# Kernel tuning notes

Hardware: AMD Instinct MI355X
Metric: run time of the kernel (lower is better)

The kernel has to match this reference:

```python
import jax, jax.numpy as jnp
import numpy as np

HEADS = 4
HID = 32
IN = 128
OUT = 8
N = 50000
E = 1600000


def setup_inputs() -> dict:
    key = jax.random.key(0)
    ks = jax.random.split(key, 12)
    x = jax.random.normal(ks[0], (N, IN), dtype=jnp.float32)
    edge_index = jax.random.randint(ks[1], (2, E), 0, N, dtype=jnp.int64)
    s = 0.05
    W1 = jax.random.normal(ks[2], (IN, HEADS * HID), dtype=jnp.float32) * s
    att_src1 = jax.random.normal(ks[3], (HEADS, HID), dtype=jnp.float32) * s
    att_dst1 = jax.random.normal(ks[4], (HEADS, HID), dtype=jnp.float32) * s
    b1 = jnp.zeros((HEADS * HID,), dtype=jnp.float32)
    W2 = jax.random.normal(ks[5], (HEADS * HID, HEADS * HID), dtype=jnp.float32) * s
    att_src2 = jax.random.normal(ks[6], (HEADS, HID), dtype=jnp.float32) * s
    att_dst2 = jax.random.normal(ks[7], (HEADS, HID), dtype=jnp.float32) * s
    b2 = jnp.zeros((HEADS * HID,), dtype=jnp.float32)
    Wout = jax.random.normal(ks[8], (HEADS * HID, OUT), dtype=jnp.float32) * s
    bout = jnp.zeros((OUT,), dtype=jnp.float32)
    return {"x": x, "edge_index": edge_index, "W1": W1, "att_src1": att_src1,
            "att_dst1": att_dst1, "b1": b1, "W2": W2, "att_src2": att_src2,
            "att_dst2": att_dst2, "b2": b2, "Wout": Wout, "bout": bout}


def gat_conv(x, src, dst, W, att_src, att_dst, b):
    n = x.shape[0]
    h = (x @ W).reshape(n, HEADS, HID)              # [N,H,C]
    a_s = (h * att_src).sum(-1)                      # [N,H]
    a_d = (h * att_dst).sum(-1)                      # [N,H]
    e = jax.nn.leaky_relu(a_s[src] + a_d[dst], 0.2)  # [E,H]
    # scatter-softmax over incoming edges of each destination node
    m = jax.ops.segment_max(e, dst, num_segments=n)
    e = jnp.exp(e - m[dst])
    denom = jax.ops.segment_sum(e, dst, num_segments=n)
    alpha = e / (denom[dst] + 1e-16)                 # [E,H]
    msg = h[src] * alpha[:, :, None]                 # [E,H,C]
    out = jax.ops.segment_sum(msg, dst, num_segments=n)
    return out.reshape(n, HEADS * HID) + b


def reference(x, edge_index, W1, att_src1, att_dst1, b1, W2, att_src2, att_dst2, b2, Wout, bout):
    n = x.shape[0]
    # GATConv adds self-loops by default
    loops = jnp.arange(n, dtype=edge_index.dtype)
    src = jnp.concatenate([edge_index[0], loops])
    dst = jnp.concatenate([edge_index[1], loops])
    # dropout p=0.6 is identity in eval mode
    h = gat_conv(x, src, dst, W1, att_src1, att_dst1, b1)
    h = jax.nn.elu(h)
    h = gat_conv(h, src, dst, W2, att_src2, att_dst2, b2)
    return h @ Wout + bout
```

## Files before the change

### kernel.cpp

```cpp
#include <hip/hip_runtime.h>
#include <hip/hip_fp16.h>
#include <math.h>

#define N_NODES 50000
#define E_EDGES 1600000
#define NE_TOT  (E_EDGES + N_NODES)

#define BSH 7
#define NBKT ((N_NODES + 127) >> 7)
#define EPW 4096
#define NWA ((NE_TOT + EPW - 1) / EPW)

#define CH 128


__global__ __launch_bounds__(256) void k_binhist(const int* __restrict__ ei,
                                                 int* __restrict__ histG) {
    __shared__ int h[NBKT];
    int t = threadIdx.x;
    for (int i = t; i < NBKT; i += 256) h[i] = 0;
    __syncthreads();
    int base = blockIdx.x * EPW;
    #pragma unroll 4
    for (int j = 0; j < EPW / 256; j++) {
        int e = base + t + 256 * j;
        if (e < NE_TOT) {
            int d = (e < E_EDGES) ? ei[E_EDGES + e] : (e - E_EDGES);
            atomicAdd(&h[d >> BSH], 1);
        }
    }
    __syncthreads();
    for (int i = t; i < NBKT; i += 256) histG[blockIdx.x * NBKT + i] = h[i];
}

__global__ __launch_bounds__(512) void k_bktscan(int* __restrict__ histG,
                                                 int* __restrict__ bktTotal) {
    __shared__ int sh[512];
    int b = blockIdx.x;
    int t = threadIdx.x;
    int v = (t < NWA) ? histG[t * NBKT + b] : 0;
    sh[t] = v;
    __syncthreads();
    for (int d = 1; d < 512; d <<= 1) {
        int x = (t >= d) ? sh[t - d] : 0;
        __syncthreads();
        sh[t] += x;
        __syncthreads();
    }
    if (t < NWA) histG[t * NBKT + b] = sh[t] - v;
    if (t == 511) bktTotal[b] = sh[511];
}

__global__ __launch_bounds__(512) void k_bktbase(const int* __restrict__ bktTotal,
                                                 int* __restrict__ bktBase,
                                                 int* __restrict__ row_start) {
    __shared__ int sc[512];
    int t = threadIdx.x;
    int v = (t < NBKT) ? bktTotal[t] : 0;
    sc[t] = v;
    __syncthreads();
    for (int d = 1; d < 512; d <<= 1) {
        int x = (t >= d) ? sc[t - d] : 0;
        __syncthreads();
        sc[t] += x;
        __syncthreads();
    }
    if (t < NBKT) bktBase[t] = sc[t] - v;
    if (t == NBKT - 1) { bktBase[NBKT] = sc[t]; row_start[N_NODES] = sc[t]; }
}

__global__ __launch_bounds__(256) void k_binscatter(const int* __restrict__ ei,
                                                    const int* __restrict__ histG,
                                                    const int* __restrict__ bktBase,
                                                    int2* __restrict__ pairs) {
    __shared__ int lofs[NBKT];
    int t = threadIdx.x;
    for (int i = t; i < NBKT; i += 256)
        lofs[i] = bktBase[i] + histG[blockIdx.x * NBKT + i];
    __syncthreads();
    int base = blockIdx.x * EPW;
    #pragma unroll 4
    for (int j = 0; j < EPW / 256; j++) {
        int e = base + t + 256 * j;
        if (e < NE_TOT) {
            int s, d;
            if (e < E_EDGES) { s = ei[e]; d = ei[E_EDGES + e]; }
            else             { s = d = e - E_EDGES; }
            int pos = atomicAdd(&lofs[d >> BSH], 1);
            pairs[pos] = make_int2(s, d);
        }
    }
}

__global__ __launch_bounds__(256) void k_bucketsort(const int2* __restrict__ pairs,
                                                    const int* __restrict__ bktBase,
                                                    int* __restrict__ row_start,
                                                    int* __restrict__ col) {
    __shared__ int cnt[1 << BSH];
    __shared__ int sc[1 << BSH];
    __shared__ int cur[1 << BSH];
    int b = blockIdx.x, t = threadIdx.x;
    int nbeg = b << BSH;
    int ebeg = bktBase[b], eend = bktBase[b + 1];
    if (t < (1 << BSH)) cnt[t] = 0;
    __syncthreads();
    for (int j = ebeg + t; j < eend; j += 256)
        atomicAdd(&cnt[pairs[j].y - nbeg], 1);
    __syncthreads();
    int v = (t < (1 << BSH)) ? cnt[t] : 0;
    if (t < (1 << BSH)) sc[t] = v;
    __syncthreads();
    for (int d = 1; d < (1 << BSH); d <<= 1) {
        int x = 0;
        if (t < (1 << BSH) && t >= d) x = sc[t - d];
        __syncthreads();
        if (t < (1 << BSH)) sc[t] += x;
        __syncthreads();
    }
    if (t < (1 << BSH)) {
        int pos = ebeg + sc[t] - v;
        cur[t] = pos;
        int node = nbeg + t;
        if (node < N_NODES) row_start[node] = pos;
    }
    __syncthreads();
    for (int j = ebeg + t; j < eend; j += 256) {
        int2 p = pairs[j];
        int pos = atomicAdd(&cur[p.y - nbeg], 1);
        col[pos] = p.x;
    }
}


__global__ __launch_bounds__(256) void k_gemm_att(
    const float* __restrict__ X, const float* __restrict__ W,
    const float* __restrict__ attS, const float* __restrict__ attD,
    __half* __restrict__ H16, float* __restrict__ a_s, float* __restrict__ a_d) {
    __shared__ float Wl[64 * 128];
    __shared__ float xs[32 * 64];
    int t = threadIdx.x;
    int g = t >> 5, cl = t & 31, c4 = cl * 4;
    int rowbase = blockIdx.x * 32;
    float4 acc[4];
    #pragma unroll
    for (int rr = 0; rr < 4; rr++) acc[rr] = make_float4(0.f, 0.f, 0.f, 0.f);

    for (int kp = 0; kp < 2; kp++) {
        __syncthreads();
        #pragma unroll
        for (int j = 0; j < 8; j++) {
            int f4 = t + 256 * j;
            int kk = f4 >> 5, cg = f4 & 31;
            *(float4*)&Wl[kk * 128 + cg * 4] =
                *(const float4*)&W[(kp * 64 + kk) * 128 + cg * 4];
        }
        #pragma unroll
        for (int j = 0; j < 2; j++) {
            int f4 = t + 256 * j;
            int r = f4 >> 4, k4 = f4 & 15;
            int grow = rowbase + r;
            float4 xv = make_float4(0.f, 0.f, 0.f, 0.f);
            if (grow < N_NODES) xv = *(const float4*)&X[grow * 128 + kp * 64 + k4 * 4];
            *(float4*)&xs[r * 64 + k4 * 4] = xv;
        }
        __syncthreads();
        #pragma unroll
        for (int k4 = 0; k4 < 16; k4++) {
            float4 xv[4];
            #pragma unroll
            for (int rr = 0; rr < 4; rr++)
                xv[rr] = *(float4*)&xs[(g * 4 + rr) * 64 + k4 * 4];
            #pragma unroll
            for (int kk = 0; kk < 4; kk++) {
                float4 wv = *(float4*)&Wl[(k4 * 4 + kk) * 128 + c4];
                #pragma unroll
                for (int rr = 0; rr < 4; rr++) {
                    float xc = (kk == 0) ? xv[rr].x : (kk == 1) ? xv[rr].y
                             : (kk == 2) ? xv[rr].z : xv[rr].w;
                    acc[rr].x += xc * wv.x;
                    acc[rr].y += xc * wv.y;
                    acc[rr].z += xc * wv.z;
                    acc[rr].w += xc * wv.w;
                }
            }
        }
    }

    float4 as4 = *(const float4*)&attS[c4];
    float4 ad4 = *(const float4*)&attD[c4];
    int head = cl >> 3;
    #pragma unroll
    for (int rr = 0; rr < 4; rr++) {
        int grow = rowbase + g * 4 + rr;
        float4 a = acc[rr];
        if (grow < N_NODES) {
            __half2 lo = __floats2half2_rn(a.x, a.y);
            __half2 hi = __floats2half2_rn(a.z, a.w);
            uint2 pk;
            pk.x = *(unsigned int*)&lo;
            pk.y = *(unsigned int*)&hi;
            *(uint2*)&H16[(size_t)grow * 128 + c4] = pk;
        }
        float ps = a.x * as4.x + a.y * as4.y + a.z * as4.z + a.w * as4.w;
        float pd = a.x * ad4.x + a.y * ad4.y + a.z * ad4.z + a.w * ad4.w;
        ps += __shfl_xor(ps, 1); ps += __shfl_xor(ps, 2); ps += __shfl_xor(ps, 4);
        pd += __shfl_xor(pd, 1); pd += __shfl_xor(pd, 2); pd += __shfl_xor(pd, 4);
        if ((cl & 7) == 0 && grow < N_NODES) {
            a_s[grow * 4 + head] = ps;
            a_d[grow * 4 + head] = pd;
        }
    }
}


__device__ inline float sel4(float4 v, int i) {
    float r = v.x;
    if (i == 1) r = v.y;
    if (i == 2) r = v.z;
    if (i == 3) r = v.w;
    return r;
}

__device__ inline float4 leaky4(float4 a, float4 b) {
    float4 e;
    e.x = a.x + b.x; e.x = e.x > 0.f ? e.x : 0.2f * e.x;
    e.y = a.y + b.y; e.y = e.y > 0.f ? e.y : 0.2f * e.y;
    e.z = a.z + b.z; e.z = e.z > 0.f ? e.z : 0.2f * e.z;
    e.w = a.w + b.w; e.w = e.w > 0.f ? e.w : 0.2f * e.w;
    return e;
}

template<int MODE>
__global__ __launch_bounds__(256) void k_agg(
    const __half* __restrict__ H16, const float* __restrict__ a_s,
    const float* __restrict__ a_d, const int* __restrict__ row_start,
    const int* __restrict__ col, const float* __restrict__ bias,
    float* __restrict__ Hout,
    const float* __restrict__ Wout, const float* __restrict__ bout,
    float* __restrict__ out) {
    __shared__ float4 eS[4][CH];
    __shared__ int    sS[4][CH];
    __shared__ float  WoT[(MODE == 0) ? 1024 : 1];
    __shared__ float  boL[(MODE == 0) ? 8 : 1];

    if (MODE == 0) {
        for (int j = threadIdx.x; j < 1024; j += 256) {
            int o = j >> 7, k = j & 127;
            WoT[o * 128 + k] = Wout[k * 8 + o];
        }
        if (threadIdx.x < 8) boL[threadIdx.x] = bout[threadIdx.x];
        __syncthreads();
    }

    int wid = threadIdx.x >> 6;
    int lane = threadIdx.x & 63;
    int node = blockIdx.x * 4 + wid;
    if (node >= N_NODES) return;
    int beg = row_start[node], end = row_start[node + 1];
    int deg = end - beg;
    float4 ad4 = *(const float4*)&a_d[node * 4];
    float4* eA = eS[wid];
    int*    srcA = sS[wid];

    float4 m = make_float4(-1e30f, -1e30f, -1e30f, -1e30f);
    for (int j = beg + lane; j < end; j += 64) {
        int src = col[j];
        float4 av = *(const float4*)&a_s[src * 4];
        float4 e = leaky4(av, ad4);
        int idx = j - beg;
        if (idx < CH) { srcA[idx] = src; eA[idx] = e; }
        m.x = fmaxf(m.x, e.x); m.y = fmaxf(m.y, e.y);
        m.z = fmaxf(m.z, e.z); m.w = fmaxf(m.w, e.w);
    }
    #pragma unroll
    for (int off = 32; off > 0; off >>= 1) {
        m.x = fmaxf(m.x, __shfl_xor(m.x, off));
        m.y = fmaxf(m.y, __shfl_xor(m.y, off));
        m.z = fmaxf(m.z, __shfl_xor(m.z, off));
        m.w = fmaxf(m.w, __shfl_xor(m.w, off));
    }

    float4 s = make_float4(0.f, 0.f, 0.f, 0.f);
    int nst = min(deg, CH);
    for (int idx = lane; idx < nst; idx += 64) {
        float4 e = eA[idx];
        float4 p;
        p.x = __expf(e.x - m.x); p.y = __expf(e.y - m.y);
        p.z = __expf(e.z - m.z); p.w = __expf(e.w - m.w);
        s.x += p.x; s.y += p.y; s.z += p.z; s.w += p.w;
        eA[idx] = p;
    }
    for (int j = beg + CH + lane; j < end; j += 64) {
        int src = col[j];
        float4 av = *(const float4*)&a_s[src * 4];
        float4 e = leaky4(av, ad4);
        s.x += __expf(e.x - m.x); s.y += __expf(e.y - m.y);
        s.z += __expf(e.z - m.z); s.w += __expf(e.w - m.w);
    }
    #pragma unroll
    for (int off = 32; off > 0; off >>= 1) {
        s.x += __shfl_xor(s.x, off);
        s.y += __shfl_xor(s.y, off);
        s.z += __shfl_xor(s.z, off);
        s.w += __shfl_xor(s.w, off);
    }
    float4 inv;
    inv.x = 1.f / (s.x + 1e-16f);
    inv.y = 1.f / (s.y + 1e-16f);
    inv.z = 1.f / (s.z + 1e-16f);
    inv.w = 1.f / (s.w + 1e-16f);

    int eslot = lane >> 4, cl16 = lane & 15, head = cl16 >> 2;
    const __half* hbase = H16 + cl16 * 8;
    const float* pA = (const float*)eA;
    float acc8[8];
    #pragma unroll
    for (int k = 0; k < 8; k++) acc8[k] = 0.f;

    #pragma unroll 4
    for (int i = eslot; i < nst; i += 4) {
        int src = srcA[i];
        float p = pA[i * 4 + head];
        float4 raw = *(const float4*)(hbase + (size_t)src * 128);
        const __half2* hp = (const __half2*)&raw;
        float2 f0 = __half22float2(hp[0]);
        float2 f1 = __half22float2(hp[1]);
        float2 f2 = __half22float2(hp[2]);
        float2 f3 = __half22float2(hp[3]);
        acc8[0] = fmaf(p, f0.x, acc8[0]); acc8[1] = fmaf(p, f0.y, acc8[1]);
        acc8[2] = fmaf(p, f1.x, acc8[2]); acc8[3] = fmaf(p, f1.y, acc8[3]);
        acc8[4] = fmaf(p, f2.x, acc8[4]); acc8[5] = fmaf(p, f2.y, acc8[5]);
        acc8[6] = fmaf(p, f3.x, acc8[6]); acc8[7] = fmaf(p, f3.y, acc8[7]);
    }
    for (int cb = beg + CH; cb < end; cb += CH) {
        int cnt = min(end - cb, CH);
        for (int idx = lane; idx < cnt; idx += 64) {
            int src = col[cb + idx];
            float4 av = *(const float4*)&a_s[src * 4];
            float4 e = leaky4(av, ad4);
            float4 p;
            p.x = __expf(e.x - m.x); p.y = __expf(e.y - m.y);
            p.z = __expf(e.z - m.z); p.w = __expf(e.w - m.w);
            srcA[idx] = src; eA[idx] = p;
        }
        #pragma unroll 4
        for (int i = eslot; i < cnt; i += 4) {
            int src = srcA[i];
            float p = pA[i * 4 + head];
            float4 raw = *(const float4*)(hbase + (size_t)src * 128);
            const __half2* hp = (const __half2*)&raw;
            float2 f0 = __half22float2(hp[0]);
            float2 f1 = __half22float2(hp[1]);
            float2 f2 = __half22float2(hp[2]);
            float2 f3 = __half22float2(hp[3]);
            acc8[0] = fmaf(p, f0.x, acc8[0]); acc8[1] = fmaf(p, f0.y, acc8[1]);
            acc8[2] = fmaf(p, f1.x, acc8[2]); acc8[3] = fmaf(p, f1.y, acc8[3]);
            acc8[4] = fmaf(p, f2.x, acc8[4]); acc8[5] = fmaf(p, f2.y, acc8[5]);
            acc8[6] = fmaf(p, f3.x, acc8[6]); acc8[7] = fmaf(p, f3.y, acc8[7]);
        }
    }

    #pragma unroll
    for (int k = 0; k < 8; k++) {
        acc8[k] += __shfl_xor(acc8[k], 16);
        acc8[k] += __shfl_xor(acc8[k], 32);
    }

    float ih = sel4(inv, head);
    if (MODE == 1) {
        if (eslot == 0) {
            const float* bp = &bias[cl16 * 8];
            float o[8];
            #pragma unroll
            for (int k = 0; k < 8; k++) {
                o[k] = acc8[k] * ih + bp[k];
                o[k] = o[k] > 0.f ? o[k] : expm1f(o[k]);
            }
            float* op = &Hout[(size_t)node * 128 + cl16 * 8];
            *(float4*)&op[0] = make_float4(o[0], o[1], o[2], o[3]);
            *(float4*)&op[4] = make_float4(o[4], o[5], o[6], o[7]);
        }
    } else {
        const float* bp = &bias[cl16 * 8];
        float4 oa, ob;
        oa.x = acc8[0] * ih + bp[0]; oa.y = acc8[1] * ih + bp[1];
        oa.z = acc8[2] * ih + bp[2]; oa.w = acc8[3] * ih + bp[3];
        ob.x = acc8[4] * ih + bp[4]; ob.y = acc8[5] * ih + bp[5];
        ob.z = acc8[6] * ih + bp[6]; ob.w = acc8[7] * ih + bp[7];
        int o0 = eslot * 2;
        float p0 = 0.f, p1 = 0.f;
        {
            float4 wa = *(float4*)&WoT[o0 * 128 + cl16 * 8];
            float4 wb = *(float4*)&WoT[o0 * 128 + cl16 * 8 + 4];
            p0 = oa.x * wa.x + oa.y * wa.y + oa.z * wa.z + oa.w * wa.w
               + ob.x * wb.x + ob.y * wb.y + ob.z * wb.z + ob.w * wb.w;
            float4 wc = *(float4*)&WoT[(o0 + 1) * 128 + cl16 * 8];
            float4 wd = *(float4*)&WoT[(o0 + 1) * 128 + cl16 * 8 + 4];
            p1 = oa.x * wc.x + oa.y * wc.y + oa.z * wc.z + oa.w * wc.w
               + ob.x * wd.x + ob.y * wd.y + ob.z * wd.z + ob.w * wd.w;
        }
        #pragma unroll
        for (int d = 1; d <= 8; d <<= 1) {
            p0 += __shfl_xor(p0, d);
            p1 += __shfl_xor(p1, d);
        }
        if (cl16 == 0) {
            float2 ov = make_float2(p0 + boL[o0], p1 + boL[o0 + 1]);
            *(float2*)&out[(size_t)node * 8 + o0] = ov;
        }
    }
}


extern "C" void kernel_launch(void* const* d_in, const int* in_sizes, int n_in,
                              void* d_out, int out_size, void* d_ws, size_t ws_size,
                              hipStream_t stream) {
    const float* x     = (const float*)d_in[0];
    const int*   ei    = (const int*)d_in[1];
    const float* W1    = (const float*)d_in[2];
    const float* attS1 = (const float*)d_in[3];
    const float* attD1 = (const float*)d_in[4];
    const float* b1    = (const float*)d_in[5];
    const float* W2    = (const float*)d_in[6];
    const float* attS2 = (const float*)d_in[7];
    const float* attD2 = (const float*)d_in[8];
    const float* b2    = (const float*)d_in[9];
    const float* Wout  = (const float*)d_in[10];
    const float* bout  = (const float*)d_in[11];
    float* out = (float*)d_out;

    char* ws = (char*)d_ws;
    size_t off = 0;
    auto alloc = [&](size_t bytes) -> void* {
        void* p = ws + off;
        off += (bytes + 255) & ~(size_t)255;
        return p;
    };
    float*  hB        = (float*)alloc((size_t)N_NODES * 128 * 4);
    __half* h16       = (__half*)alloc((size_t)N_NODES * 128 * 2);
    float*  a_s       = (float*)alloc((size_t)N_NODES * 4 * 4);
    float*  a_d       = (float*)alloc((size_t)N_NODES * 4 * 4);
    int*    row_start = (int*)alloc((size_t)(N_NODES + 1) * 4);
    int*    col       = (int*)alloc((size_t)NE_TOT * 4);
    int*    histG     = (int*)alloc((size_t)NWA * NBKT * 4);
    int*    bktTotal  = (int*)alloc((size_t)NBKT * 4);
    int*    bktBase   = (int*)alloc((size_t)(NBKT + 1) * 4);
    int2*   pairs     = (int2*)hB;

    k_binhist<<<NWA, 256, 0, stream>>>(ei, histG);
    k_bktscan<<<NBKT, 512, 0, stream>>>(histG, bktTotal);
    k_bktbase<<<1, 512, 0, stream>>>(bktTotal, bktBase, row_start);
    k_binscatter<<<NWA, 256, 0, stream>>>(ei, histG, bktBase, pairs);
    k_bucketsort<<<NBKT, 256, 0, stream>>>(pairs, bktBase, row_start, col);

    int nbG = (N_NODES + 31) / 32;
    int nbA = (N_NODES + 3) / 4;
    k_gemm_att<<<nbG, 256, 0, stream>>>(x, W1, attS1, attD1, h16, a_s, a_d);
    k_agg<1><<<nbA, 256, 0, stream>>>(h16, a_s, a_d, row_start, col, b1, hB,
                                      Wout, bout, out);
    k_gemm_att<<<nbG, 256, 0, stream>>>(hB, W2, attS2, attD2, h16, a_s, a_d);
    k_agg<0><<<nbA, 256, 0, stream>>>(h16, a_s, a_d, row_start, col, b2, hB,
                                      Wout, bout, out);
}
```

Baseline: 271.5 us.

## Co-launch edge histogram with first-layer GEMM and unroll gather loop

Merges the edge-bucket histogram pass and the layer-1 feature GEMM into one launch. Block indices below NWA run the histogram and the remaining blocks run the GEMM, sharing one 40 KB shared-memory buffer. This removes a launch and lets two independent stages run at the same time. Separately, the first aggregation chunk loop is hand-unrolled to issue four independent row gathers before accumulating, to expose more memory-level parallelism. The larger shared allocation for histogram blocks and the extra registers may lower occupancy.

Result: no change. 268.5 us (-1.1%).

```diff
diff --git a/kernel.cpp b/kernel.cpp
--- a/kernel.cpp
+++ b/kernel.cpp
@@ -14,133 +14,13 @@
 #define CH 128
 
 
-__global__ __launch_bounds__(256) void k_binhist(const int* __restrict__ ei,
-                                                 int* __restrict__ histG) {
-    __shared__ int h[NBKT];
-    int t = threadIdx.x;
-    for (int i = t; i < NBKT; i += 256) h[i] = 0;
-    __syncthreads();
-    int base = blockIdx.x * EPW;
-    #pragma unroll 4
-    for (int j = 0; j < EPW / 256; j++) {
-        int e = base + t + 256 * j;
-        if (e < NE_TOT) {
-            int d = (e < E_EDGES) ? ei[E_EDGES + e] : (e - E_EDGES);
-            atomicAdd(&h[d >> BSH], 1);
-        }
-    }
-    __syncthreads();
-    for (int i = t; i < NBKT; i += 256) histG[blockIdx.x * NBKT + i] = h[i];
-}
-
-__global__ __launch_bounds__(512) void k_bktscan(int* __restrict__ histG,
-                                                 int* __restrict__ bktTotal) {
-    __shared__ int sh[512];
-    int b = blockIdx.x;
-    int t = threadIdx.x;
-    int v = (t < NWA) ? histG[t * NBKT + b] : 0;
-    sh[t] = v;
-    __syncthreads();
-    for (int d = 1; d < 512; d <<= 1) {
-        int x = (t >= d) ? sh[t - d] : 0;
-        __syncthreads();
-        sh[t] += x;
-        __syncthreads();
-    }
-    if (t < NWA) histG[t * NBKT + b] = sh[t] - v;
-    if (t == 511) bktTotal[b] = sh[511];
-}
-
-__global__ __launch_bounds__(512) void k_bktbase(const int* __restrict__ bktTotal,
-                                                 int* __restrict__ bktBase,
-                                                 int* __restrict__ row_start) {
-    __shared__ int sc[512];
-    int t = threadIdx.x;
-    int v = (t < NBKT) ? bktTotal[t] : 0;
-    sc[t] = v;
-    __syncthreads();
-    for (int d = 1; d < 512; d <<= 1) {
-        int x = (t >= d) ? sc[t - d] : 0;
-        __syncthreads();
-        sc[t] += x;
-        __syncthreads();
-    }
-    if (t < NBKT) bktBase[t] = sc[t] - v;
-    if (t == NBKT - 1) { bktBase[NBKT] = sc[t]; row_start[N_NODES] = sc[t]; }
-}
-
-__global__ __launch_bounds__(256) void k_binscatter(const int* __restrict__ ei,
-                                                    const int* __restrict__ histG,
-                                                    const int* __restrict__ bktBase,
-                                                    int2* __restrict__ pairs) {
-    __shared__ int lofs[NBKT];
-    int t = threadIdx.x;
-    for (int i = t; i < NBKT; i += 256)
-        lofs[i] = bktBase[i] + histG[blockIdx.x * NBKT + i];
-    __syncthreads();
-    int base = blockIdx.x * EPW;
-    #pragma unroll 4
-    for (int j = 0; j < EPW / 256; j++) {
-        int e = base + t + 256 * j;
-        if (e < NE_TOT) {
-            int s, d;
-            if (e < E_EDGES) { s = ei[e]; d = ei[E_EDGES + e]; }
-            else             { s = d = e - E_EDGES; }
-            int pos = atomicAdd(&lofs[d >> BSH], 1);
-            pairs[pos] = make_int2(s, d);
-        }
-    }
-}
-
-__global__ __launch_bounds__(256) void k_bucketsort(const int2* __restrict__ pairs,
-                                                    const int* __restrict__ bktBase,
-                                                    int* __restrict__ row_start,
-                                                    int* __restrict__ col) {
-    __shared__ int cnt[1 << BSH];
-    __shared__ int sc[1 << BSH];
-    __shared__ int cur[1 << BSH];
-    int b = blockIdx.x, t = threadIdx.x;
-    int nbeg = b << BSH;
-    int ebeg = bktBase[b], eend = bktBase[b + 1];
-    if (t < (1 << BSH)) cnt[t] = 0;
-    __syncthreads();
-    for (int j = ebeg + t; j < eend; j += 256)
-        atomicAdd(&cnt[pairs[j].y - nbeg], 1);
-    __syncthreads();
-    int v = (t < (1 << BSH)) ? cnt[t] : 0;
-    if (t < (1 << BSH)) sc[t] = v;
-    __syncthreads();
-    for (int d = 1; d < (1 << BSH); d <<= 1) {
-        int x = 0;
-        if (t < (1 << BSH) && t >= d) x = sc[t - d];
-        __syncthreads();
-        if (t < (1 << BSH)) sc[t] += x;
-        __syncthreads();
-    }
-    if (t < (1 << BSH)) {
-        int pos = ebeg + sc[t] - v;
-        cur[t] = pos;
-        int node = nbeg + t;
-        if (node < N_NODES) row_start[node] = pos;
-    }
-    __syncthreads();
-    for (int j = ebeg + t; j < eend; j += 256) {
-        int2 p = pairs[j];
-        int pos = atomicAdd(&cur[p.y - nbeg], 1);
-        col[pos] = p.x;
-    }
-}
-
-
-__global__ __launch_bounds__(256) void k_gemm_att(
+__device__ __forceinline__ void gemm_att_body(
+    int bid, int t, float* Wl, float* xs,
     const float* __restrict__ X, const float* __restrict__ W,
     const float* __restrict__ attS, const float* __restrict__ attD,
     __half* __restrict__ H16, float* __restrict__ a_s, float* __restrict__ a_d) {
-    __shared__ float Wl[64 * 128];
-    __shared__ float xs[32 * 64];
-    int t = threadIdx.x;
     int g = t >> 5, cl = t & 31, c4 = cl * 4;
-    int rowbase = blockIdx.x * 32;
+    int rowbase = bid * 32;
     float4 acc[4];
     #pragma unroll
     for (int rr = 0; rr < 4; rr++) acc[rr] = make_float4(0.f, 0.f, 0.f, 0.f);
@@ -212,6 +92,143 @@
     }
 }
 
+__global__ __launch_bounds__(256) void k_hist_gemm(
+    const int* __restrict__ ei, int* __restrict__ histG,
+    const float* __restrict__ X, const float* __restrict__ W,
+    const float* __restrict__ attS, const float* __restrict__ attD,
+    __half* __restrict__ H16, float* __restrict__ a_s, float* __restrict__ a_d) {
+    __shared__ __align__(16) char smem[40960];
+    int t = threadIdx.x;
+    if (blockIdx.x < NWA) {
+        int* h = (int*)smem;
+        for (int i = t; i < NBKT; i += 256) h[i] = 0;
+        __syncthreads();
+        int base = blockIdx.x * EPW;
+        #pragma unroll 4
+        for (int j = 0; j < EPW / 256; j++) {
+            int e = base + t + 256 * j;
+            if (e < NE_TOT) {
+                int d = (e < E_EDGES) ? ei[E_EDGES + e] : (e - E_EDGES);
+                atomicAdd(&h[d >> BSH], 1);
+            }
+        }
+        __syncthreads();
+        for (int i = t; i < NBKT; i += 256) histG[blockIdx.x * NBKT + i] = h[i];
+    } else {
+        float* Wl = (float*)smem;
+        float* xs = (float*)(smem + 32768);
+        gemm_att_body(blockIdx.x - NWA, t, Wl, xs, X, W, attS, attD, H16, a_s, a_d);
+    }
+}
+
+__global__ __launch_bounds__(256) void k_gemm_att(
+    const float* __restrict__ X, const float* __restrict__ W,
+    const float* __restrict__ attS, const float* __restrict__ attD,
+    __half* __restrict__ H16, float* __restrict__ a_s, float* __restrict__ a_d) {
+    __shared__ float Wl[64 * 128];
+    __shared__ float xs[32 * 64];
+    gemm_att_body(blockIdx.x, threadIdx.x, Wl, xs, X, W, attS, attD, H16, a_s, a_d);
+}
+
+
+__global__ __launch_bounds__(512) void k_bktscan(int* __restrict__ histG,
+                                                 int* __restrict__ bktTotal) {
+    __shared__ int sh[512];
+    int b = blockIdx.x;
+    int t = threadIdx.x;
+    int v = (t < NWA) ? histG[t * NBKT + b] : 0;
+    sh[t] = v;
+    __syncthreads();
+    for (int d = 1; d < 512; d <<= 1) {
+        int x = (t >= d) ? sh[t - d] : 0;
+        __syncthreads();
+        sh[t] += x;
+        __syncthreads();
+    }
+    if (t < NWA) histG[t * NBKT + b] = sh[t] - v;
+    if (t == 511) bktTotal[b] = sh[511];
+}
+
+__global__ __launch_bounds__(512) void k_bktbase(const int* __restrict__ bktTotal,
+                                                 int* __restrict__ bktBase,
+                                                 int* __restrict__ row_start) {
+    __shared__ int sc[512];
+    int t = threadIdx.x;
+    int v = (t < NBKT) ? bktTotal[t] : 0;
+    sc[t] = v;
+    __syncthreads();
+    for (int d = 1; d < 512; d <<= 1) {
+        int x = (t >= d) ? sc[t - d] : 0;
+        __syncthreads();
+        sc[t] += x;
+        __syncthreads();
+    }
+    if (t < NBKT) bktBase[t] = sc[t] - v;
+    if (t == NBKT - 1) { bktBase[NBKT] = sc[t]; row_start[N_NODES] = sc[t]; }
+}
+
+__global__ __launch_bounds__(256) void k_binscatter(const int* __restrict__ ei,
+                                                    const int* __restrict__ histG,
+                                                    const int* __restrict__ bktBase,
+                                                    int2* __restrict__ pairs) {
+    __shared__ int lofs[NBKT];
+    int t = threadIdx.x;
+    for (int i = t; i < NBKT; i += 256)
+        lofs[i] = bktBase[i] + histG[blockIdx.x * NBKT + i];
+    __syncthreads();
+    int base = blockIdx.x * EPW;
+    #pragma unroll 4
+    for (int j = 0; j < EPW / 256; j++) {
+        int e = base + t + 256 * j;
+        if (e < NE_TOT) {
+            int s, d;
+            if (e < E_EDGES) { s = ei[e]; d = ei[E_EDGES + e]; }
+            else             { s = d = e - E_EDGES; }
+            int pos = atomicAdd(&lofs[d >> BSH], 1);
+            pairs[pos] = make_int2(s, d);
+        }
+    }
+}
+
+__global__ __launch_bounds__(256) void k_bucketsort(const int2* __restrict__ pairs,
+                                                    const int* __restrict__ bktBase,
+                                                    int* __restrict__ row_start,
+                                                    int* __restrict__ col) {
+    __shared__ int cnt[1 << BSH];
+    __shared__ int sc[1 << BSH];
+    __shared__ int cur[1 << BSH];
+    int b = blockIdx.x, t = threadIdx.x;
+    int nbeg = b << BSH;
+    int ebeg = bktBase[b], eend = bktBase[b + 1];
+    if (t < (1 << BSH)) cnt[t] = 0;
+    __syncthreads();
+    for (int j = ebeg + t; j < eend; j += 256)
+        atomicAdd(&cnt[pairs[j].y - nbeg], 1);
+    __syncthreads();
+    int v = (t < (1 << BSH)) ? cnt[t] : 0;
+    if (t < (1 << BSH)) sc[t] = v;
+    __syncthreads();
+    for (int d = 1; d < (1 << BSH); d <<= 1) {
+        int x = 0;
+        if (t < (1 << BSH) && t >= d) x = sc[t - d];
+        __syncthreads();
+        if (t < (1 << BSH)) sc[t] += x;
+        __syncthreads();
+    }
+    if (t < (1 << BSH)) {
+        int pos = ebeg + sc[t] - v;
+        cur[t] = pos;
+        int node = nbeg + t;
+        if (node < N_NODES) row_start[node] = pos;
+    }
+    __syncthreads();
+    for (int j = ebeg + t; j < eend; j += 256) {
+        int2 p = pairs[j];
+        int pos = atomicAdd(&cur[p.y - nbeg], 1);
+        col[pos] = p.x;
+    }
+}
+
 
 __device__ inline float sel4(float4 v, int i) {
     float r = v.x;
@@ -229,6 +246,23 @@
     e.w = a.w + b.w; e.w = e.w > 0.f ? e.w : 0.2f * e.w;
     return e;
 }
+
+#define ACC8(q, raw)                                              \
+    do {                                                          \
+        const __half2* hp_ = (const __half2*)&(raw);              \
+        float2 f0_ = __half22float2(hp_[0]);                      \
+        float2 f1_ = __half22float2(hp_[1]);                      \
+        float2 f2_ = __half22float2(hp_[2]);                      \
+        float2 f3_ = __half22float2(hp_[3]);                      \
+        acc8[0] = fmaf((q), f0_.x, acc8[0]);                      \
+        acc8[1] = fmaf((q), f0_.y, acc8[1]);                      \
+        acc8[2] = fmaf((q), f1_.x, acc8[2]);                      \
+        acc8[3] = fmaf((q), f1_.y, acc8[3]);                      \
+        acc8[4] = fmaf((q), f2_.x, acc8[4]);                      \
+        acc8[5] = fmaf((q), f2_.y, acc8[5]);                      \
+        acc8[6] = fmaf((q), f3_.x, acc8[6]);                      \
+        acc8[7] = fmaf((q), f3_.y, acc8[7]);                      \
+    } while (0)
 
 template<int MODE>
 __global__ __launch_bounds__(256) void k_agg(
@@ -317,20 +351,30 @@
     #pragma unroll
     for (int k = 0; k < 8; k++) acc8[k] = 0.f;
 
-    #pragma unroll 4
-    for (int i = eslot; i < nst; i += 4) {
+    int i = eslot;
+    for (; i + 12 < nst; i += 16) {
+        int s0 = srcA[i];
+        int s1 = srcA[i + 4];
+        int s2 = srcA[i + 8];
+        int s3 = srcA[i + 12];
+        float q0 = pA[i * 4 + head];
+        float q1 = pA[(i + 4) * 4 + head];
+        float q2 = pA[(i + 8) * 4 + head];
+        float q3 = pA[(i + 12) * 4 + head];
+        float4 r0 = *(const float4*)(hbase + (size_t)s0 * 128);
+        float4 r1 = *(const float4*)(hbase + (size_t)s1 * 128);
+        float4 r2 = *(const float4*)(hbase + (size_t)s2 * 128);
+        float4 r3 = *(const float4*)(hbase + (size_t)s3 * 128);
+        ACC8(q0, r0);
+        ACC8(q1, r1);
+        ACC8(q2, r2);
+        ACC8(q3, r3);
+    }
+    for (; i < nst; i += 4) {
         int src = srcA[i];
         float p = pA[i * 4 + head];
         float4 raw = *(const float4*)(hbase + (size_t)src * 128);
-        const __half2* hp = (const __half2*)&raw;
-        float2 f0 = __half22float2(hp[0]);
-        float2 f1 = __half22float2(hp[1]);
-        float2 f2 = __half22float2(hp[2]);
-        float2 f3 = __half22float2(hp[3]);
-        acc8[0] = fmaf(p, f0.x, acc8[0]); acc8[1] = fmaf(p, f0.y, acc8[1]);
-        acc8[2] = fmaf(p, f1.x, acc8[2]); acc8[3] = fmaf(p, f1.y, acc8[3]);
-        acc8[4] = fmaf(p, f2.x, acc8[4]); acc8[5] = fmaf(p, f2.y, acc8[5]);
-        acc8[6] = fmaf(p, f3.x, acc8[6]); acc8[7] = fmaf(p, f3.y, acc8[7]);
+        ACC8(p, raw);
     }
     for (int cb = beg + CH; cb < end; cb += CH) {
         int cnt = min(end - cb, CH);
@@ -343,20 +387,11 @@
             p.z = __expf(e.z - m.z); p.w = __expf(e.w - m.w);
             srcA[idx] = src; eA[idx] = p;
         }
-        #pragma unroll 4
-        for (int i = eslot; i < cnt; i += 4) {
-            int src = srcA[i];
-            float p = pA[i * 4 + head];
+        for (int ii = eslot; ii < cnt; ii += 4) {
+            int src = srcA[ii];
+            float p = pA[ii * 4 + head];
             float4 raw = *(const float4*)(hbase + (size_t)src * 128);
-            const __half2* hp = (const __half2*)&raw;
-            float2 f0 = __half22float2(hp[0]);
-            float2 f1 = __half22float2(hp[1]);
-            float2 f2 = __half22float2(hp[2]);
-            float2 f3 = __half22float2(hp[3]);
-            acc8[0] = fmaf(p, f0.x, acc8[0]); acc8[1] = fmaf(p, f0.y, acc8[1]);
-            acc8[2] = fmaf(p, f1.x, acc8[2]); acc8[3] = fmaf(p, f1.y, acc8[3]);
-            acc8[4] = fmaf(p, f2.x, acc8[4]); acc8[5] = fmaf(p, f2.y, acc8[5]);
-            acc8[6] = fmaf(p, f3.x, acc8[6]); acc8[7] = fmaf(p, f3.y, acc8[7]);
+            ACC8(p, raw);
         }
     }
 
@@ -447,15 +482,16 @@
     int*    bktBase   = (int*)alloc((size_t)(NBKT + 1) * 4);
     int2*   pairs     = (int2*)hB;
 
-    k_binhist<<<NWA, 256, 0, stream>>>(ei, histG);
+    int nbG = (N_NODES + 31) / 32;
+    int nbA = (N_NODES + 3) / 4;
+
+    k_hist_gemm<<<NWA + nbG, 256, 0, stream>>>(ei, histG, x, W1, attS1, attD1,
+                                               h16, a_s, a_d);
     k_bktscan<<<NBKT, 512, 0, stream>>>(histG, bktTotal);
     k_bktbase<<<1, 512, 0, stream>>>(bktTotal, bktBase, row_start);
     k_binscatter<<<NWA, 256, 0, stream>>>(ei, histG, bktBase, pairs);
     k_bucketsort<<<NBKT, 256, 0, stream>>>(pairs, bktBase, row_start, col);
 
-    int nbG = (N_NODES + 31) / 32;
-    int nbA = (N_NODES + 3) / 4;
-    k_gemm_att<<<nbG, 256, 0, stream>>>(x, W1, attS1, attD1, h16, a_s, a_d);
     k_agg<1><<<nbA, 256, 0, stream>>>(h16, a_s, a_d, row_start, col, b1, hB,
                                       Wout, bout, out);
     k_gemm_att<<<nbG, 256, 0, stream>>>(hB, W2, attS2, attD2, h16, a_s, a_d);
```
